# Kernel tuning notes

Hardware: AMD Instinct MI355X
Metric: run time of the kernel (lower is better)

## Reference

```python
import jax, jax.numpy as jnp
import numpy as np

N, E, D, H, ED = 50000, 150000, 128, 4, 16


def _ln(x, g, b, eps=1e-5):
    m = jnp.mean(x, -1, keepdims=True)
    v = jnp.var(x, -1, keepdims=True)
    return (x - m) / jnp.sqrt(v + eps) * g + b


def _seg_softmax(logits, seg, n):
    # numerically stable softmax over edges grouped by destination node
    m = jax.ops.segment_max(logits, seg, num_segments=n)
    e = jnp.exp(logits - m[seg])
    s = jax.ops.segment_sum(e, seg, num_segments=n)
    return e / (s[seg] + 1e-16)


def setup_inputs():
    key = jax.random.key(0)
    ks = jax.random.split(key, 16)
    def w(i, shape, s=0.05):
        return jax.random.normal(ks[i], shape, jnp.float32) * s
    return dict(
        x=w(0, (N, D), 1.0),
        edge_index=jax.random.randint(ks[1], (2, E), 0, N),
        edge_attr=w(2, (E, ED), 1.0),
        sage_Wl=w(3, (D, D)), sage_Wr=w(4, (D, D)), sage_b=jnp.zeros((D,), jnp.float32),
        tq_W=w(5, (D, H * D)), tq_b=jnp.zeros((H * D,), jnp.float32),
        tk_W=w(6, (D, H * D)), tk_b=jnp.zeros((H * D,), jnp.float32),
        tv_W=w(7, (D, H * D)), tv_b=jnp.zeros((H * D,), jnp.float32),
        te_W=w(8, (ED, H * D)),
        tskip_W=w(9, (D, D)), tskip_b=jnp.zeros((D,), jnp.float32),
        gat_W=w(10, (D, H * D)), gat_att_src=w(11, (H, D)), gat_att_dst=w(12, (H, D)),
        gat_bias=jnp.zeros((D,), jnp.float32),
        gate_short=jnp.ones((1,), jnp.float32), gate_attn=jnp.ones((1,), jnp.float32),
        gate_neighbor=jnp.ones((1,), jnp.float32),
        fus_W=w(13, (3 * D, D)), fus_b=jnp.zeros((D,), jnp.float32),
        fus_g=jnp.ones((D,), jnp.float32), fus_beta=jnp.zeros((D,), jnp.float32),
        norm_g=jnp.ones((D,), jnp.float32), norm_b=jnp.zeros((D,), jnp.float32),
    )


def reference(x, edge_index, edge_attr, sage_Wl, sage_Wr, sage_b,
              tq_W, tq_b, tk_W, tk_b, tv_W, tv_b, te_W, tskip_W, tskip_b,
              gat_W, gat_att_src, gat_att_dst, gat_bias,
              gate_short, gate_attn, gate_neighbor,
              fus_W, fus_b, fus_g, fus_beta, norm_g, norm_b):
    n, d = x.shape
    h = tq_W.shape[1] // d
    src, dst = edge_index[0], edge_index[1]

    # --- SAGEConv: mean aggregation of neighbors + root linear ---
    agg = jax.ops.segment_sum(x[src], dst, num_segments=n)
    cnt = jax.ops.segment_sum(jnp.ones((src.shape[0],), x.dtype), dst, num_segments=n)
    mean = agg / jnp.maximum(cnt, 1.0)[:, None]
    x_short = jax.nn.relu(mean @ sage_Wl + x @ sage_Wr + sage_b)

    # --- TransformerConv (concat=False, edge-conditioned key/value, skip) ---
    q = (x @ tq_W + tq_b).reshape(n, h, d)
    k = (x @ tk_W + tk_b).reshape(n, h, d)
    v = (x @ tv_W + tv_b).reshape(n, h, d)
    e = (edge_attr @ te_W).reshape(-1, h, d)           # [E,H,d]
    logits = jnp.sum(q[dst] * (k[src] + e), -1) / np.float32(np.sqrt(d))  # [E,H]
    alpha = _seg_softmax(logits, dst, n)
    out_t = jax.ops.segment_sum((v[src] + e) * alpha[..., None], dst, num_segments=n).mean(1)
    x_attn = jax.nn.relu(out_t + x @ tskip_W + tskip_b)

    # --- GATConv (adds self-loops, concat=False averages heads, bias) ---
    loops = jnp.arange(n)
    s2 = jnp.concatenate([src, loops])
    d2 = jnp.concatenate([dst, loops])
    g = (x @ gat_W).reshape(n, h, d)
    a_s = jnp.sum(g * gat_att_src, -1)                 # [N,H]
    a_d = jnp.sum(g * gat_att_dst, -1)
    lg = jax.nn.leaky_relu(a_s[s2] + a_d[d2], 0.2)     # [E+N,H]
    al = _seg_softmax(lg, d2, n)
    out_g = jax.ops.segment_sum(g[s2] * al[..., None], d2, num_segments=n).mean(1) + gat_bias
    x_nb = jax.nn.relu(out_g)

    # --- gated fusion + residual LayerNorm ---
    gs = jax.nn.sigmoid(gate_short)
    ga = jax.nn.sigmoid(gate_attn)
    gn = jax.nn.sigmoid(gate_neighbor)
    cat = jnp.concatenate([x_short * gs, x_attn * ga, x_nb * gn], -1)
    fused = jax.nn.relu(_ln(cat @ fus_W + fus_b, fus_g, fus_beta))
    return _ln(x + fused, norm_g, norm_b)
```

## Files before the change

kernel.cpp:

```cpp
#include <hip/hip_runtime.h>
#include <hip/hip_bf16.h>

using bf16 = __hip_bfloat16;
typedef __attribute__((ext_vector_type(8))) short short8;
typedef __attribute__((ext_vector_type(4))) float f32x4;
typedef __attribute__((ext_vector_type(4))) unsigned short u16x4;

__device__ __forceinline__ void store4(bf16* p, float v0, float v1, float v2, float v3) {
    u16x4 pk;
    bf16 h0 = __float2bfloat16(v0); pk[0] = *(unsigned short*)&h0;
    bf16 h1 = __float2bfloat16(v1); pk[1] = *(unsigned short*)&h1;
    bf16 h2 = __float2bfloat16(v2); pk[2] = *(unsigned short*)&h2;
    bf16 h3 = __float2bfloat16(v3); pk[3] = *(unsigned short*)&h3;
    *(u16x4*)p = pk;
}
__device__ __forceinline__ float b2f(short s) { bf16 h; *(short*)&h = s; return __bfloat162float(h); }

__device__ __forceinline__ void ld_lds16(void* lds, const void* g) {
    __builtin_amdgcn_global_load_lds(
        (const __attribute__((address_space(1))) unsigned int*)g,
        (__attribute__((address_space(3))) unsigned int*)lds,
        16, 0, 0);
}

__device__ __forceinline__ size_t pidx(int c, int k, int K) {
    return ((size_t)(((c >> 6) * (K >> 5) + (k >> 5)) * 4 + ((c >> 4) & 3)) * 64
            + (((k >> 3) & 3) * 16 + (c & 15))) * 8 + (k & 7);
}

__global__ __launch_bounds__(256) void zero_ws(unsigned* p, size_t n) {
    size_t i = (size_t)blockIdx.x * 256 + threadIdx.x;
    size_t stride = (size_t)gridDim.x * 256;
    for (; i < n; i += stride) p[i] = 0u;
}

__global__ __launch_bounds__(256) void prep_all(
    const float* __restrict__ x, bf16* __restrict__ x_b,
    bf16* __restrict__ Wt_sage, const float* __restrict__ sage_Wl, const float* __restrict__ sage_Wr,
    bf16* __restrict__ Wt_fus, const float* __restrict__ fus_W,
    const float* __restrict__ gate_s, const float* __restrict__ gate_a, const float* __restrict__ gate_n,
    bf16* __restrict__ Wt_cat, const float* __restrict__ tvW,
    const float* __restrict__ tskipW, const float* __restrict__ teW,
    bf16* __restrict__ Wgag, const float* __restrict__ gatW,
    float* __restrict__ bvsum, const float* __restrict__ tvb, int ND)
{
    const int TP = 128 * 128;
    long i = (long)blockIdx.x * 256 + threadIdx.x;
    long nv = ND >> 3;
    if (i < nv) {
        long b = i * 8;
        f32x4 a0 = *(const f32x4*)(x + b);
        f32x4 a1 = *(const f32x4*)(x + b + 4);
        short8 o;
        #pragma unroll
        for (int j = 0; j < 4; ++j) { bf16 h = __float2bfloat16(a0[j]); o[j] = *(short*)&h; }
        #pragma unroll
        for (int j = 0; j < 4; ++j) { bf16 h = __float2bfloat16(a1[j]); o[4 + j] = *(short*)&h; }
        *(short8*)(x_b + b) = o;
        return;
    }
    i -= nv;
    if (i < TP) { int k = (int)i / 128, c = (int)i % 128; Wt_sage[pidx(c, k, 256)] = __float2bfloat16(sage_Wl[i]); return; }
    i -= TP;
    if (i < TP) { int k = (int)i / 128, c = (int)i % 128; Wt_sage[pidx(c, k + 128, 256)] = __float2bfloat16(sage_Wr[i]); return; }
    i -= TP;
    if (i < 3 * TP) {
        int sseg = (int)(i / TP); int r = (int)(i % TP);
        int k = r / 128, c = r % 128;
        const float* g = sseg == 0 ? gate_s : (sseg == 1 ? gate_a : gate_n);
        float gv = 1.0f / (1.0f + expf(-g[0]));
        Wt_fus[pidx(c, sseg * 128 + k, 384)] = __float2bfloat16(fus_W[(size_t)sseg * TP + r] * gv);
        return;
    }
    i -= 3L * TP;
    if (i < 128L * 704) {
        int d = (int)(i / 704), kk = (int)(i % 704);
        float v;
        if (kk < 512)      { int h = kk >> 7, k = kk & 127; v = 0.25f * tvW[k * 512 + h * 128 + d]; }
        else if (kk < 640) { int k = kk - 512;              v = tskipW[k * 128 + d]; }
        else               { int t = kk - 640; int h = t >> 4, j = t & 15; v = 0.25f * teW[j * 512 + h * 128 + d]; }
        Wt_cat[pidx(d, kk, 704)] = __float2bfloat16(v);
        return;
    }
    i -= 128L * 704;
    if (i < 128L * 512) {
        int d = (int)i >> 9, k = (int)i & 511;
        int h = k >> 7, i2 = k & 127;
        Wgag[pidx(d, k, 512)] = __float2bfloat16(0.25f * gatW[(size_t)i2 * 512 + h * 128 + d]);
        return;
    }
    i -= 128L * 512;
    if (i < 128) {
        int d = (int)i;
        bvsum[d] = 0.25f * (tvb[d] + tvb[128 + d] + tvb[256 + d] + tvb[384 + d]);
    }
}

__global__ __launch_bounds__(128) void build_wbig(
    bf16* __restrict__ Wbig, float* __restrict__ bbig,
    const float* __restrict__ Wq, const float* __restrict__ Wk,
    const float* __restrict__ teW, const float* __restrict__ bq,
    const float* __restrict__ bk, const float* __restrict__ gatW,
    const float* __restrict__ attS, const float* __restrict__ attD)
{
    int c = blockIdx.x;
    int ip = threadIdx.x;
    float acc = 0.f, bacc = 0.f;
    if (c < 512) {
        int h = c >> 7, i2 = c & 127;
        const float* wkrow = Wk + (size_t)i2 * 512 + h * 128;
        const float* wqrow = Wq + (size_t)ip * 512 + h * 128;
        for (int o = 0; o < 128; ++o) acc += wqrow[o] * wkrow[o];
        if (ip == 0) { const float* bqr = bq + h * 128; for (int o = 0; o < 128; ++o) bacc += bqr[o] * wkrow[o]; }
    } else if (c < 576) {
        int t = c - 512; int h = t >> 4, j = t & 15;
        const float* terow = teW + (size_t)j * 512 + h * 128;
        const float* wqrow = Wq + (size_t)ip * 512 + h * 128;
        for (int o = 0; o < 128; ++o) acc += wqrow[o] * terow[o];
        if (ip == 0) { const float* bqr = bq + h * 128; for (int o = 0; o < 128; ++o) bacc += bqr[o] * terow[o]; }
    } else if (c < 580) {
        int h = c - 576;
        const float* bkr = bk + h * 128;
        const float* wqrow = Wq + (size_t)ip * 512 + h * 128;
        for (int o = 0; o < 128; ++o) acc += wqrow[o] * bkr[o];
        if (ip == 0) { const float* bqr = bq + h * 128; for (int o = 0; o < 128; ++o) bacc += bqr[o] * bkr[o]; }
    } else if (c < 584) {
        int h = c - 580;
        const float* ar = attS + h * 128;
        const float* gr = gatW + (size_t)ip * 512 + h * 128;
        for (int d = 0; d < 128; ++d) acc += gr[d] * ar[d];
    } else if (c < 588) {
        int h = c - 584;
        const float* ar = attD + h * 128;
        const float* gr = gatW + (size_t)ip * 512 + h * 128;
        for (int d = 0; d < 128; ++d) acc += gr[d] * ar[d];
    }
    Wbig[pidx(c, ip, 128)] = __float2bfloat16(acc);
    if (ip == 0) bbig[c] = bacc;
}

__global__ __launch_bounds__(256) void k_hist(const int* __restrict__ dst, int* __restrict__ deg_i, int E) {
    int e = blockIdx.x * 256 + threadIdx.x;
    if (e < E) atomicAdd(&deg_i[dst[e]], 1);
}

__global__ __launch_bounds__(256) void k_scan1(
    const int* __restrict__ deg_i, int* __restrict__ loc, int* __restrict__ partial, int N)
{
    __shared__ int sm[256];
    int t = threadIdx.x, i = blockIdx.x * 256 + t;
    int v = (i < N) ? deg_i[i] : 0;
    sm[t] = v;
    __syncthreads();
    for (int off = 1; off < 256; off <<= 1) {
        int add = (t >= off) ? sm[t - off] : 0;
        __syncthreads();
        sm[t] += add;
        __syncthreads();
    }
    if (i < N) loc[i] = sm[t] - v;
    if (t == 255) partial[blockIdx.x] = sm[255];
}

__global__ __launch_bounds__(256) void k_scan2(int* __restrict__ partial, int nb) {
    __shared__ int sm[256];
    int t = threadIdx.x;
    int v = (t < nb) ? partial[t] : 0;
    sm[t] = v;
    __syncthreads();
    for (int off = 1; off < 256; off <<= 1) {
        int add = (t >= off) ? sm[t - off] : 0;
        __syncthreads();
        sm[t] += add;
        __syncthreads();
    }
    if (t < nb) partial[t] = sm[t] - v;
}

__global__ __launch_bounds__(256) void k_scan3(
    const int* __restrict__ loc, const int* __restrict__ partial,
    int* __restrict__ rowptr, int* __restrict__ cursor, int N)
{
    int i = blockIdx.x * 256 + threadIdx.x;
    if (i >= N) return;
    int r = loc[i] + partial[blockIdx.x];
    rowptr[i] = r;
    cursor[i] = r;
}

__global__ __launch_bounds__(256) void k_scatter(
    const int* __restrict__ src, const int* __restrict__ dst,
    int* __restrict__ cursor, int* __restrict__ col_src, int* __restrict__ eidx, int E)
{
    int e = blockIdx.x * 256 + threadIdx.x;
    if (e >= E) return;
    int d = dst[e];
    int pos = atomicAdd(&cursor[d], 1);
    col_src[pos] = src[e];
    eidx[pos] = e;
}

__global__ __launch_bounds__(128) void gemm_wide(
    const bf16* __restrict__ A, const bf16* __restrict__ Wt,
    const float* __restrict__ bias, bf16* __restrict__ C, int n_rows, int ldc)
{
    int row0 = blockIdx.x * 64;
    int wave = threadIdx.x >> 6, lane = threadIdx.x & 63;
    int lrow = lane & 15, quad = lane >> 4;
    short8 xb[4][4];
    #pragma unroll
    for (int ks = 0; ks < 4; ++ks)
        #pragma unroll
        for (int nt = 0; nt < 4; ++nt) {
            int r = row0 + nt * 16 + lrow;
            r = r < n_rows ? r : n_rows - 1;
            xb[ks][nt] = *(const short8*)(A + (size_t)r * 128 + ks * 32 + quad * 8);
        }
    int c64 = blockIdx.y * 2 + wave;
    int cbase = c64 * 64;
    f32x4 acc[4][4] = {};
    #pragma unroll
    for (int ks = 0; ks < 4; ++ks) {
        short8 wf[4];
        #pragma unroll
        for (int mt = 0; mt < 4; ++mt)
            wf[mt] = *(const short8*)(Wt + ((size_t)((c64 * 4 + ks) * 4 + mt) * 64 + lane) * 8);
        #pragma unroll
        for (int mt = 0; mt < 4; ++mt)
            #pragma unroll
            for (int nt = 0; nt < 4; ++nt)
                acc[mt][nt] = __builtin_amdgcn_mfma_f32_16x16x32_bf16(wf[mt], xb[ks][nt], acc[mt][nt], 0, 0, 0);
    }
    #pragma unroll
    for (int nt = 0; nt < 4; ++nt) {
        int row = row0 + nt * 16 + lrow;
        if (row >= n_rows) continue;
        #pragma unroll
        for (int mt = 0; mt < 4; ++mt) {
            int col = cbase + mt * 16 + quad * 4;
            float b0 = 0.f, b1 = 0.f, b2 = 0.f, b3 = 0.f;
            if (bias) { b0 = bias[col]; b1 = bias[col + 1]; b2 = bias[col + 2]; b3 = bias[col + 3]; }
            store4(&C[(size_t)row * ldc + col],
                   acc[mt][nt][0] + b0, acc[mt][nt][1] + b1,
                   acc[mt][nt][2] + b2, acc[mt][nt][3] + b3);
        }
    }
}

#define NCAP 8
__global__ __launch_bounds__(256) void node_fused(
    const bf16* __restrict__ QT, const bf16* __restrict__ x_b,
    const float* __restrict__ edge_attr,
    const int* __restrict__ rowptr, const int* __restrict__ deg_i,
    const int* __restrict__ col_src, const int* __restrict__ eidx,
    bf16* __restrict__ mean_b, bf16* __restrict__ xa, bf16* __restrict__ ga,
    bf16* __restrict__ ea_b, int N)
{
    __shared__ short8 xS[4][NCAP][16];
    __shared__ float eaS[4][NCAP][16];
    __shared__ float wTs[4][NCAP][4];
    __shared__ float wGs[4][NCAP][4];
    int w = threadIdx.x >> 6, l = threadIdx.x & 63;
    int n = blockIdx.x * 4 + w;
    if (n >= N) return;
    int j = l & 15, g4 = l >> 4;
    int p0 = rowptr[n], dg = deg_i[n];
    const float scale = 0.08838834764831845f;
    float qtF[4][8], qeqL[4], qbL[4], adh[4], ashn[4];
    #pragma unroll
    for (int h = 0; h < 4; ++h) {
        short8 q = *(const short8*)(QT + (size_t)n * 640 + h * 128 + j * 8);
        #pragma unroll
        for (int t = 0; t < 8; ++t) qtF[h][t] = b2f(q[t]);
        qeqL[h] = __bfloat162float(QT[(size_t)n * 640 + 512 + h * 16 + j]);
        qbL[h]  = __bfloat162float(QT[(size_t)n * 640 + 576 + h]);
        ashn[h] = __bfloat162float(QT[(size_t)n * 640 + 580 + h]);
        adh[h]  = __bfloat162float(QT[(size_t)n * 640 + 584 + h]);
    }
    float xn0 = __bfloat162float(x_b[(size_t)n * 128 + l]);
    float xn1 = __bfloat162float(x_b[(size_t)n * 128 + l + 64]);
    float s_t[4], s_g[4], xaacc[8] = {}, gaacc[8];
    float mean0 = 0.f, mean1 = 0.f, eaacc = 0.f;
    #pragma unroll
    for (int h = 0; h < 4; ++h) {
        s_t[h] = 0.f;
        float lgs = ashn[h] + adh[h];
        lgs = lgs > 0.f ? lgs : 0.2f * lgs;
        float e = __expf(lgs);
        s_g[h] = e;
        gaacc[h * 2] = e * xn0; gaacc[h * 2 + 1] = e * xn1;
    }
    for (int c0 = 0; c0 < dg; c0 += NCAP) {
        int cc = min(NCAP, dg - c0);
        for (int it = 0; it < ((cc + 3) >> 2); ++it) {
            int i = it * 4 + g4;
            bool valid = i < cc;
            int s = 0;
            short8 xf = {0, 0, 0, 0, 0, 0, 0, 0};
            float ea_j = 0.f;
            if (valid) {
                s = col_src[p0 + c0 + i];
                int eg = eidx[p0 + c0 + i];
                xf = *(const short8*)(x_b + (size_t)s * 128 + j * 8);
                ea_j = edge_attr[(size_t)eg * 16 + j];
                xS[w][i][j] = xf;
                eaS[w][i][j] = ea_j;
            }
            float xv[8];
            #pragma unroll
            for (int t = 0; t < 8; ++t) xv[t] = b2f(xf[t]);
            float p[4];
            #pragma unroll
            for (int h = 0; h < 4; ++h) {
                float a = ea_j * qeqL[h];
                #pragma unroll
                for (int t = 0; t < 8; ++t) a += xv[t] * qtF[h][t];
                p[h] = a;
            }
            #pragma unroll
            for (int off = 1; off < 16; off <<= 1)
                #pragma unroll
                for (int h = 0; h < 4; ++h)
                    p[h] += __shfl_xor(p[h], off, 64);
            if (valid && j == 0) {
                #pragma unroll
                for (int h = 0; h < 4; ++h) {
                    wTs[w][i][h] = __expf((p[h] + qbL[h]) * scale);
                    float as_s = __bfloat162float(QT[(size_t)s * 640 + 580 + h]);
                    float lg = as_s + adh[h];
                    lg = lg > 0.f ? lg : 0.2f * lg;
                    wGs[w][i][h] = __expf(lg);
                }
            }
        }
        for (int i = 0; i < cc; ++i) {
            const bf16* xr = (const bf16*)&xS[w][i][0];
            float xv0 = __bfloat162float(xr[l]);
            float xv1 = __bfloat162float(xr[l + 64]);
            mean0 += xv0; mean1 += xv1;
            #pragma unroll
            for (int h = 0; h < 4; ++h) {
                float at = wTs[w][i][h], ag = wGs[w][i][h];
                s_t[h] += at; s_g[h] += ag;
                xaacc[h * 2] += at * xv0; xaacc[h * 2 + 1] += at * xv1;
                gaacc[h * 2] += ag * xv0; gaacc[h * 2 + 1] += ag * xv1;
            }
            eaacc += wTs[w][i][g4] * eaS[w][i][j];
        }
    }
    float invd = 1.f / fmaxf((float)dg, 1.f);
    mean_b[(size_t)n * 128 + l]      = __float2bfloat16(mean0 * invd);
    mean_b[(size_t)n * 128 + l + 64] = __float2bfloat16(mean1 * invd);
    #pragma unroll
    for (int h = 0; h < 4; ++h) {
        float it = 1.f / (s_t[h] + 1e-16f);
        xa[(size_t)n * 512 + h * 128 + l]      = __float2bfloat16(xaacc[h * 2] * it);
        xa[(size_t)n * 512 + h * 128 + l + 64] = __float2bfloat16(xaacc[h * 2 + 1] * it);
        float ig = 1.f / (s_g[h] + 1e-16f);
        ga[(size_t)n * 512 + h * 128 + l]      = __float2bfloat16(gaacc[h * 2] * ig);
        ga[(size_t)n * 512 + h * 128 + l + 64] = __float2bfloat16(gaacc[h * 2 + 1] * ig);
    }
    ea_b[(size_t)n * 64 + l] = __float2bfloat16(eaacc / (s_t[g4] + 1e-16f));
}

#define STASH(BIASP, USE_BV) do { \
    _Pragma("unroll") \
    for (int nt = 0; nt < 4; ++nt) { \
        int row_l = nt * 16 + lrow; \
        int sw = (row_l & 7) << 4; \
        float bvf = (USE_BV) ? ((deg_i[rA[nt]] > 0) ? 1.f : 0.f) : 0.f; \
        _Pragma("unroll") \
        for (int mt = 0; mt < 4; ++mt) { \
            int col = cbase + mt * 16 + quad * 4; \
            f32x4 bb = *(const f32x4*)((BIASP) + col); \
            u16x4 pk; \
            _Pragma("unroll") \
            for (int jj = 0; jj < 4; ++jj) { \
                float v = acc[mt][nt][jj] + bb[jj]; \
                if (USE_BV) v += bvf * bvsum[col + jj]; \
                bf16 h = __float2bfloat16(fmaxf(v, 0.f)); \
                pk[jj] = *(unsigned short*)&h; \
            } \
            *(u16x4*)(tileb + row_l * 256 + ((col * 2) ^ sw)) = pk; \
        } \
    } \
} while (0)

__global__ __launch_bounds__(128) void tail_fused(
    const bf16* __restrict__ mean_b, const bf16* __restrict__ x_b,
    const bf16* __restrict__ ga, const bf16* __restrict__ xa,
    const bf16* __restrict__ ea_b, const int* __restrict__ deg_i,
    const float* __restrict__ x,
    const bf16* __restrict__ Wt_sage, const bf16* __restrict__ Wgag,
    const bf16* __restrict__ Wt_cat, const bf16* __restrict__ Wt_fus,
    const float* __restrict__ sage_b, const float* __restrict__ gat_bias,
    const float* __restrict__ tskip_b, const float* __restrict__ bvsum,
    const float* __restrict__ fus_b, const float* __restrict__ fus_g,
    const float* __restrict__ fus_beta, const float* __restrict__ norm_g,
    const float* __restrict__ norm_b,
    float* __restrict__ out, int N)
{
    __shared__ __align__(16) char tileb[64 * 256];
    __shared__ __align__(16) short8 stg[2][2][8][64];
    __shared__ float2 st1[2][64];
    __shared__ float2 st2[2][64];
    int wave = threadIdx.x >> 6, lane = threadIdx.x & 63;
    int lrow = lane & 15, quad = lane >> 4;
    int kq = quad * 8;
    int row0 = blockIdx.x * 64;
    int cbase = wave * 64;
    int rA[4];
    #pragma unroll
    for (int t = 0; t < 4; ++t) {
        int r = row0 + t * 16 + lrow;
        rA[t] = r < N ? r : N - 1;
    }
    f32x4 facc[4][4] = {};

    auto issueA = [&](const bf16* base, int ldA, int kA, int par) {
        #pragma unroll
        for (int t = 0; t < 4; ++t)
            ld_lds16(&stg[wave][par][t][0], base + (size_t)rA[t] * ldA + kA);
    };
    auto issueW = [&](const bf16* Wt, int stepIdx, int par) {
        #pragma unroll
        for (int mt = 0; mt < 4; ++mt)
            ld_lds16(&stg[wave][par][4 + mt][0], Wt + ((size_t)(stepIdx * 4 + mt) * 64 + lane) * 8);
    };
    auto mfstep = [&](f32x4 (&acc)[4][4], int par) {
        short8 xf[4], wf[4];
        #pragma unroll
        for (int t = 0; t < 4; ++t) { xf[t] = stg[wave][par][t][lane]; wf[t] = stg[wave][par][4 + t][lane]; }
        #pragma unroll
        for (int mt = 0; mt < 4; ++mt)
            #pragma unroll
            for (int nt = 0; nt < 4; ++nt)
                acc[mt][nt] = __builtin_amdgcn_mfma_f32_16x16x32_bf16(wf[mt], xf[nt], acc[mt][nt], 0, 0, 0);
    };
    auto fuse_seg = [&](int SEG) {
        issueW(Wt_fus, wave * 12 + SEG * 4, 0);
        issueW(Wt_fus, wave * 12 + SEG * 4 + 1, 1);
        #pragma unroll
        for (int ks = 0; ks < 4; ++ks) {
            int cur = ks & 1;
            if (ks < 3) asm volatile("s_waitcnt vmcnt(4)" ::: "memory");
            else        asm volatile("s_waitcnt vmcnt(0)" ::: "memory");
            int kT = ks * 32 + kq;
            short8 xf[4], wf[4];
            #pragma unroll
            for (int t = 0; t < 4; ++t) {
                int row_l = t * 16 + lrow;
                xf[t] = *(const short8*)(tileb + row_l * 256 + ((kT * 2) ^ ((row_l & 7) << 4)));
            }
            #pragma unroll
            for (int mt = 0; mt < 4; ++mt) wf[mt] = stg[wave][cur][4 + mt][lane];
            #pragma unroll
            for (int mt = 0; mt < 4; ++mt)
                #pragma unroll
                for (int nt = 0; nt < 4; ++nt)
                    facc[mt][nt] = __builtin_amdgcn_mfma_f32_16x16x32_bf16(wf[mt], xf[nt], facc[mt][nt], 0, 0, 0);
            if (ks + 2 < 4) {
                asm volatile("s_waitcnt lgkmcnt(0)" ::: "memory");
                issueW(Wt_fus, wave * 12 + SEG * 4 + ks + 2, cur);
            }
        }
    };

    {
        f32x4 acc[4][4] = {};
        issueA(mean_b, 128, kq, 0);
        issueW(Wt_sage, wave * 8, 0);
        issueA(mean_b, 128, 32 + kq, 1);
        issueW(Wt_sage, wave * 8 + 1, 1);
        #pragma unroll
        for (int ks = 0; ks < 8; ++ks) {
            int cur = ks & 1;
            if (ks < 7) asm volatile("s_waitcnt vmcnt(8)" ::: "memory");
            else        asm volatile("s_waitcnt vmcnt(0)" ::: "memory");
            mfstep(acc, cur);
            if (ks + 2 < 8) {
                asm volatile("s_waitcnt lgkmcnt(0)" ::: "memory");
                int p = ks + 2;
                issueA((p < 4) ? mean_b : x_b, 128, (p & 3) * 32 + kq, cur);
                issueW(Wt_sage, wave * 8 + p, cur);
            }
        }
        STASH(sage_b, 0);
    }
    __syncthreads();
    fuse_seg(0);
    __syncthreads();

    {
        f32x4 acc[4][4] = {};
        issueA(xa, 512, kq, 0);
        issueW(Wt_cat, wave * 22, 0);
        issueA(xa, 512, 32 + kq, 1);
        issueW(Wt_cat, wave * 22 + 1, 1);
        #pragma unroll
        for (int ks = 0; ks < 22; ++ks) {
            int cur = ks & 1;
            if (ks < 21) asm volatile("s_waitcnt vmcnt(8)" ::: "memory");
            else         asm volatile("s_waitcnt vmcnt(0)" ::: "memory");
            mfstep(acc, cur);
            if (ks + 2 < 22) {
                asm volatile("s_waitcnt lgkmcnt(0)" ::: "memory");
                int p = ks + 2;
                if (p < 16)      issueA(xa,   512, p * 32 + kq,        cur);
                else if (p < 20) issueA(x_b,  128, (p - 16) * 32 + kq, cur);
                else             issueA(ea_b,  64, (p - 20) * 32 + kq, cur);
                issueW(Wt_cat, wave * 22 + p, cur);
            }
        }
        STASH(tskip_b, 1);
    }
    __syncthreads();
    fuse_seg(1);
    __syncthreads();

    {
        f32x4 acc[4][4] = {};
        issueA(ga, 512, kq, 0);
        issueW(Wgag, wave * 16, 0);
        issueA(ga, 512, 32 + kq, 1);
        issueW(Wgag, wave * 16 + 1, 1);
        #pragma unroll
        for (int ks = 0; ks < 16; ++ks) {
            int cur = ks & 1;
            if (ks < 15) asm volatile("s_waitcnt vmcnt(8)" ::: "memory");
            else         asm volatile("s_waitcnt vmcnt(0)" ::: "memory");
            mfstep(acc, cur);
            if (ks + 2 < 16) {
                asm volatile("s_waitcnt lgkmcnt(0)" ::: "memory");
                int p = ks + 2;
                issueA(ga, 512, p * 32 + kq, cur);
                issueW(Wgag, wave * 16 + p, cur);
            }
        }
        STASH(gat_bias, 0);
    }
    __syncthreads();
    fuse_seg(2);

    #pragma unroll
    for (int nt = 0; nt < 4; ++nt) {
        float s = 0.f, q = 0.f;
        #pragma unroll
        for (int mt = 0; mt < 4; ++mt) {
            int col = cbase + mt * 16 + quad * 4;
            f32x4 bb = *(const f32x4*)(fus_b + col);
            #pragma unroll
            for (int jj = 0; jj < 4; ++jj) {
                float v = facc[mt][nt][jj] + bb[jj];
                facc[mt][nt][jj] = v;
                s += v; q += v * v;
            }
        }
        s += __shfl_xor(s, 16, 64); q += __shfl_xor(q, 16, 64);
        s += __shfl_xor(s, 32, 64); q += __shfl_xor(q, 32, 64);
        if (quad == 0) st1[wave][nt * 16 + lrow] = make_float2(s, q);
    }
    __syncthreads();
    float m1[4], inv1[4];
    #pragma unroll
    for (int nt = 0; nt < 4; ++nt) {
        float2 a = st1[0][nt * 16 + lrow], b = st1[1][nt * 16 + lrow];
        float S = a.x + b.x, Q = a.y + b.y;
        float m = S * (1.f / 128.f);
        m1[nt] = m;
        inv1[nt] = rsqrtf(Q * (1.f / 128.f) - m * m + 1e-5f);
    }
    #pragma unroll
    for (int nt = 0; nt < 4; ++nt) {
        float s = 0.f, q = 0.f;
        #pragma unroll
        for (int mt = 0; mt < 4; ++mt) {
            int col = cbase + mt * 16 + quad * 4;
            f32x4 gv = *(const f32x4*)(fus_g + col);
            f32x4 bv = *(const f32x4*)(fus_beta + col);
            f32x4 xv = *(const f32x4*)(x + (size_t)rA[nt] * 128 + col);
            #pragma unroll
            for (int jj = 0; jj < 4; ++jj) {
                float y = fmaxf((facc[mt][nt][jj] - m1[nt]) * inv1[nt] * gv[jj] + bv[jj], 0.f);
                float z = xv[jj] + y;
                facc[mt][nt][jj] = z;
                s += z; q += z * z;
            }
        }
        s += __shfl_xor(s, 16, 64); q += __shfl_xor(q, 16, 64);
        s += __shfl_xor(s, 32, 64); q += __shfl_xor(q, 32, 64);
        if (quad == 0) st2[wave][nt * 16 + lrow] = make_float2(s, q);
    }
    __syncthreads();
    #pragma unroll
    for (int nt = 0; nt < 4; ++nt) {
        int row = row0 + nt * 16 + lrow;
        if (row >= N) continue;
        float2 a = st2[0][nt * 16 + lrow], b = st2[1][nt * 16 + lrow];
        float S = a.x + b.x, Q = a.y + b.y;
        float m = S * (1.f / 128.f);
        float inv = rsqrtf(Q * (1.f / 128.f) - m * m + 1e-5f);
        #pragma unroll
        for (int mt = 0; mt < 4; ++mt) {
            int col = cbase + mt * 16 + quad * 4;
            f32x4 ngv = *(const f32x4*)(norm_g + col);
            f32x4 nbv = *(const f32x4*)(norm_b + col);
            f32x4 o;
            #pragma unroll
            for (int jj = 0; jj < 4; ++jj)
                o[jj] = (facc[mt][nt][jj] - m) * inv * ngv[jj] + nbv[jj];
            *(f32x4*)(out + (size_t)row * 128 + col) = o;
        }
    }
}

extern "C" void kernel_launch(void* const* d_in, const int* in_sizes, int n_in,
                              void* d_out, int out_size, void* d_ws, size_t ws_size,
                              hipStream_t stream)
{
    const float* x        = (const float*)d_in[0];
    const int*   ei       = (const int*)d_in[1];
    const float* edge_attr= (const float*)d_in[2];
    const float* sage_Wl  = (const float*)d_in[3];
    const float* sage_Wr  = (const float*)d_in[4];
    const float* sage_b   = (const float*)d_in[5];
    const float* tq_W     = (const float*)d_in[6];
    const float* tq_b     = (const float*)d_in[7];
    const float* tk_W     = (const float*)d_in[8];
    const float* tk_b     = (const float*)d_in[9];
    const float* tv_W     = (const float*)d_in[10];
    const float* tv_b     = (const float*)d_in[11];
    const float* te_W     = (const float*)d_in[12];
    const float* tskip_W  = (const float*)d_in[13];
    const float* tskip_b  = (const float*)d_in[14];
    const float* gat_W    = (const float*)d_in[15];
    const float* att_s_w  = (const float*)d_in[16];
    const float* att_d_w  = (const float*)d_in[17];
    const float* gat_bias = (const float*)d_in[18];
    const float* gate_s   = (const float*)d_in[19];
    const float* gate_a   = (const float*)d_in[20];
    const float* gate_n   = (const float*)d_in[21];
    const float* fus_W    = (const float*)d_in[22];
    const float* fus_b    = (const float*)d_in[23];
    const float* fus_g    = (const float*)d_in[24];
    const float* fus_beta = (const float*)d_in[25];
    const float* norm_g   = (const float*)d_in[26];
    const float* norm_b   = (const float*)d_in[27];

    int N = in_sizes[0] / 128;
    int E = in_sizes[2] / 16;
    const int* src = ei;
    const int* dst = ei + E;
    int ND = N * 128;
    int nb = (N + 255) / 256;

    char* wsb = (char*)d_ws;
    size_t off = 0;
    auto carve = [&](size_t bytes) -> char* {
        char* p = wsb + off;
        off += (bytes + 255) & ~(size_t)255;
        return p;
    };
    int*   deg_i   = (int*)carve((size_t)N * 4);
    size_t zero_bytes = off;
    int*   rowptr  = (int*)carve((size_t)N * 4);
    int*   cursor  = (int*)carve((size_t)N * 4);
    int*   loc     = (int*)carve((size_t)N * 4);
    int*   partial = (int*)carve((size_t)256 * 4);
    int*   col_src = (int*)carve((size_t)E * 4);
    int*   eidx    = (int*)carve((size_t)E * 4);
    bf16*  x_b     = (bf16*)carve((size_t)N * 128 * 2);
    bf16*  QT      = (bf16*)carve((size_t)N * 640 * 2);
    bf16*  xa      = (bf16*)carve((size_t)N * 512 * 2);
    bf16*  ga      = (bf16*)carve((size_t)N * 512 * 2);
    bf16*  mean_b  = (bf16*)carve((size_t)N * 128 * 2);
    bf16*  ea_b    = (bf16*)carve((size_t)N * 64 * 2);
    bf16*  Wbig    = (bf16*)carve((size_t)640 * 128 * 2);
    float* bbig    = (float*)carve((size_t)640 * 4);
    bf16*  Wt_sage = (bf16*)carve((size_t)128 * 256 * 2);
    bf16*  Wt_fus  = (bf16*)carve((size_t)128 * 384 * 2);
    bf16*  Wt_cat  = (bf16*)carve((size_t)128 * 704 * 2);
    bf16*  Wgag    = (bf16*)carve((size_t)128 * 512 * 2);
    float* bvsum   = (float*)carve((size_t)128 * 4);

    zero_ws<<<256, 256, 0, stream>>>((unsigned*)wsb, zero_bytes / 4);
    const long TP = 128 * 128;
    long prep_total = (long)(ND >> 3) + 5L * TP + 128L * 704 + 128L * 512 + 128;
    int prep_blocks = (int)((prep_total + 255) / 256);
    prep_all<<<prep_blocks, 256, 0, stream>>>(
        x, x_b, Wt_sage, sage_Wl, sage_Wr, Wt_fus, fus_W, gate_s, gate_a, gate_n,
        Wt_cat, tv_W, tskip_W, te_W, Wgag, gat_W, bvsum, tv_b, ND);
    build_wbig<<<640, 128, 0, stream>>>(Wbig, bbig, tq_W, tk_W, te_W, tq_b, tk_b,
                                        gat_W, att_s_w, att_d_w);

    k_hist<<<(E + 255) / 256, 256, 0, stream>>>(dst, deg_i, E);
    k_scan1<<<nb, 256, 0, stream>>>(deg_i, loc, partial, N);
    k_scan2<<<1, 256, 0, stream>>>(partial, nb);
    k_scan3<<<nb, 256, 0, stream>>>(loc, partial, rowptr, cursor, N);
    k_scatter<<<(E + 255) / 256, 256, 0, stream>>>(src, dst, cursor, col_src, eidx, E);

    int gy64 = (N + 63) / 64, gnode = (N + 3) / 4;

    gemm_wide<<<dim3(gy64, 5), 128, 0, stream>>>(x_b, Wbig, bbig, QT, N, 640);

    node_fused<<<gnode, 256, 0, stream>>>(QT, x_b, edge_attr, rowptr, deg_i, col_src, eidx,
                                          mean_b, xa, ga, ea_b, N);

    tail_fused<<<gy64, 128, 0, stream>>>(
        mean_b, x_b, ga, xa, ea_b, deg_i, x,
        Wt_sage, Wgag, Wt_cat, Wt_fus,
        sage_b, gat_bias, tskip_b, bvsum,
        fus_b, fus_g, fus_beta, norm_g, norm_b,
        (float*)d_out, N);
}
```

Baseline: 373.4 us.

## Fold weight-build and zeroing into prep kernel; loop gemm_wide over column tiles with LDS prefetch

The separate zero_ws and build_wbig launches are removed. Their work, the Wbig/bbig fold and zeroing the degree histogram, now runs as extra index ranges inside prep_all, which cuts two kernel launches. gemm_wide now uses a 1D grid: each block keeps its x fragments in registers and loops over all five 128-column groups. Weight tiles are double-buffered into LDS with global_load_lds and manual waitcnt. This reuses the A loads across column groups and hides weight fetch latency, at the cost of fewer blocks, less parallelism and per-thread serial dot products now inside prep_all.

```diff
diff --git a/kernel.cpp b/kernel.cpp
--- a/kernel.cpp
+++ b/kernel.cpp
@@ -26,12 +26,6 @@
 __device__ __forceinline__ size_t pidx(int c, int k, int K) {
     return ((size_t)(((c >> 6) * (K >> 5) + (k >> 5)) * 4 + ((c >> 4) & 3)) * 64
             + (((k >> 3) & 3) * 16 + (c & 15))) * 8 + (k & 7);
-}
-
-__global__ __launch_bounds__(256) void zero_ws(unsigned* p, size_t n) {
-    size_t i = (size_t)blockIdx.x * 256 + threadIdx.x;
-    size_t stride = (size_t)gridDim.x * 256;
-    for (; i < n; i += stride) p[i] = 0u;
 }
 
 __global__ __launch_bounds__(256) void prep_all(
@@ -42,7 +36,12 @@
     bf16* __restrict__ Wt_cat, const float* __restrict__ tvW,
     const float* __restrict__ tskipW, const float* __restrict__ teW,
     bf16* __restrict__ Wgag, const float* __restrict__ gatW,
-    float* __restrict__ bvsum, const float* __restrict__ tvb, int ND)
+    float* __restrict__ bvsum, const float* __restrict__ tvb,
+    bf16* __restrict__ Wbig, float* __restrict__ bbig,
+    const float* __restrict__ Wq, const float* __restrict__ Wk,
+    const float* __restrict__ bq, const float* __restrict__ bk,
+    const float* __restrict__ attS, const float* __restrict__ attD,
+    int* __restrict__ deg_i, int N, int ND)
 {
     const int TP = 128 * 128;
     long i = (long)blockIdx.x * 256 + threadIdx.x;
@@ -93,57 +92,57 @@
     if (i < 128) {
         int d = (int)i;
         bvsum[d] = 0.25f * (tvb[d] + tvb[128 + d] + tvb[256 + d] + tvb[384 + d]);
-    }
-}
-
-__global__ __launch_bounds__(128) void build_wbig(
-    bf16* __restrict__ Wbig, float* __restrict__ bbig,
-    const float* __restrict__ Wq, const float* __restrict__ Wk,
-    const float* __restrict__ teW, const float* __restrict__ bq,
-    const float* __restrict__ bk, const float* __restrict__ gatW,
-    const float* __restrict__ attS, const float* __restrict__ attD)
-{
-    int c = blockIdx.x;
-    int ip = threadIdx.x;
-    float acc = 0.f, bacc = 0.f;
-    if (c < 512) {
-        int h = c >> 7, i2 = c & 127;
-        const float* wkrow = Wk + (size_t)i2 * 512 + h * 128;
-        const float* wqrow = Wq + (size_t)ip * 512 + h * 128;
-        for (int o = 0; o < 128; ++o) acc += wqrow[o] * wkrow[o];
-        if (ip == 0) { const float* bqr = bq + h * 128; for (int o = 0; o < 128; ++o) bacc += bqr[o] * wkrow[o]; }
-    } else if (c < 576) {
-        int t = c - 512; int h = t >> 4, j = t & 15;
-        const float* terow = teW + (size_t)j * 512 + h * 128;
-        const float* wqrow = Wq + (size_t)ip * 512 + h * 128;
-        for (int o = 0; o < 128; ++o) acc += wqrow[o] * terow[o];
-        if (ip == 0) { const float* bqr = bq + h * 128; for (int o = 0; o < 128; ++o) bacc += bqr[o] * terow[o]; }
-    } else if (c < 580) {
-        int h = c - 576;
-        const float* bkr = bk + h * 128;
-        const float* wqrow = Wq + (size_t)ip * 512 + h * 128;
-        for (int o = 0; o < 128; ++o) acc += wqrow[o] * bkr[o];
-        if (ip == 0) { const float* bqr = bq + h * 128; for (int o = 0; o < 128; ++o) bacc += bqr[o] * bkr[o]; }
-    } else if (c < 584) {
-        int h = c - 580;
-        const float* ar = attS + h * 128;
-        const float* gr = gatW + (size_t)ip * 512 + h * 128;
-        for (int d = 0; d < 128; ++d) acc += gr[d] * ar[d];
-    } else if (c < 588) {
-        int h = c - 584;
-        const float* ar = attD + h * 128;
-        const float* gr = gatW + (size_t)ip * 512 + h * 128;
-        for (int d = 0; d < 128; ++d) acc += gr[d] * ar[d];
-    }
-    Wbig[pidx(c, ip, 128)] = __float2bfloat16(acc);
-    if (ip == 0) bbig[c] = bacc;
+        return;
+    }
+    i -= 128;
+    if (i < 640L * 128) {
+        int c = (int)(i >> 7), ip = (int)(i & 127);
+        float acc = 0.f, bacc = 0.f;
+        if (c < 512) {
+            int h = c >> 7, i2 = c & 127;
+            const float* wkrow = Wk + (size_t)i2 * 512 + h * 128;
+            const float* wqrow = Wq + (size_t)ip * 512 + h * 128;
+            for (int o = 0; o < 128; ++o) acc += wqrow[o] * wkrow[o];
+            if (ip == 0) { const float* bqr = bq + h * 128; for (int o = 0; o < 128; ++o) bacc += bqr[o] * wkrow[o]; }
+        } else if (c < 576) {
+            int t = c - 512; int h = t >> 4, j = t & 15;
+            const float* terow = teW + (size_t)j * 512 + h * 128;
+            const float* wqrow = Wq + (size_t)ip * 512 + h * 128;
+            for (int o = 0; o < 128; ++o) acc += wqrow[o] * terow[o];
+            if (ip == 0) { const float* bqr = bq + h * 128; for (int o = 0; o < 128; ++o) bacc += bqr[o] * terow[o]; }
+        } else if (c < 580) {
+            int h = c - 576;
+            const float* bkr = bk + h * 128;
+            const float* wqrow = Wq + (size_t)ip * 512 + h * 128;
+            for (int o = 0; o < 128; ++o) acc += wqrow[o] * bkr[o];
+            if (ip == 0) { const float* bqr = bq + h * 128; for (int o = 0; o < 128; ++o) bacc += bqr[o] * bkr[o]; }
+        } else if (c < 584) {
+            int h = c - 580;
+            const float* ar = attS + h * 128;
+            const float* gr = gatW + (size_t)ip * 512 + h * 128;
+            for (int d = 0; d < 128; ++d) acc += gr[d] * ar[d];
+        } else if (c < 588) {
+            int h = c - 584;
+            const float* ar = attD + h * 128;
+            const float* gr = gatW + (size_t)ip * 512 + h * 128;
+            for (int d = 0; d < 128; ++d) acc += gr[d] * ar[d];
+        }
+        Wbig[pidx(c, ip, 128)] = __float2bfloat16(acc);
+        if (ip == 0) bbig[c] = bacc;
+        return;
+    }
+    i -= 640L * 128;
+    long z = i * 4;
+    if (z < N) {
+        if (z + 4 <= N) { *(int4*)(deg_i + z) = make_int4(0, 0, 0, 0); }
+        else { for (long zz = z; zz < N; ++zz) deg_i[zz] = 0; }
+    }
 }
 
 __global__ __launch_bounds__(256) void k_hist(const int* __restrict__ dst, int* __restrict__ deg_i, int E) {
     int e = blockIdx.x * 256 + threadIdx.x;
     if (e < E) atomicAdd(&deg_i[dst[e]], 1);
 }
-
 __global__ __launch_bounds__(256) void k_scan1(
     const int* __restrict__ deg_i, int* __restrict__ loc, int* __restrict__ partial, int N)
 {
@@ -161,7 +160,6 @@
     if (i < N) loc[i] = sm[t] - v;
     if (t == 255) partial[blockIdx.x] = sm[255];
 }
-
 __global__ __launch_bounds__(256) void k_scan2(int* __restrict__ partial, int nb) {
     __shared__ int sm[256];
     int t = threadIdx.x;
@@ -176,7 +174,6 @@
     }
     if (t < nb) partial[t] = sm[t] - v;
 }
-
 __global__ __launch_bounds__(256) void k_scan3(
     const int* __restrict__ loc, const int* __restrict__ partial,
     int* __restrict__ rowptr, int* __restrict__ cursor, int N)
@@ -187,7 +184,6 @@
     rowptr[i] = r;
     cursor[i] = r;
 }
-
 __global__ __launch_bounds__(256) void k_scatter(
     const int* __restrict__ src, const int* __restrict__ dst,
     int* __restrict__ cursor, int* __restrict__ col_src, int* __restrict__ eidx, int E)
@@ -204,6 +200,7 @@
     const bf16* __restrict__ A, const bf16* __restrict__ Wt,
     const float* __restrict__ bias, bf16* __restrict__ C, int n_rows, int ldc)
 {
+    __shared__ __align__(16) short8 wstg[2][2][4][64];
     int row0 = blockIdx.x * 64;
     int wave = threadIdx.x >> 6, lane = threadIdx.x & 63;
     int lrow = lane & 15, quad = lane >> 4;
@@ -216,33 +213,47 @@
             r = r < n_rows ? r : n_rows - 1;
             xb[ks][nt] = *(const short8*)(A + (size_t)r * 128 + ks * 32 + quad * 8);
         }
-    int c64 = blockIdx.y * 2 + wave;
-    int cbase = c64 * 64;
-    f32x4 acc[4][4] = {};
-    #pragma unroll
-    for (int ks = 0; ks < 4; ++ks) {
-        short8 wf[4];
+    auto issueW = [&](int s, int par) {
+        int c64 = (s >> 2) * 2 + wave, ks = s & 3;
         #pragma unroll
         for (int mt = 0; mt < 4; ++mt)
-            wf[mt] = *(const short8*)(Wt + ((size_t)((c64 * 4 + ks) * 4 + mt) * 64 + lane) * 8);
-        #pragma unroll
-        for (int mt = 0; mt < 4; ++mt)
-            #pragma unroll
-            for (int nt = 0; nt < 4; ++nt)
-                acc[mt][nt] = __builtin_amdgcn_mfma_f32_16x16x32_bf16(wf[mt], xb[ks][nt], acc[mt][nt], 0, 0, 0);
-    }
-    #pragma unroll
-    for (int nt = 0; nt < 4; ++nt) {
-        int row = row0 + nt * 16 + lrow;
-        if (row >= n_rows) continue;
-        #pragma unroll
-        for (int mt = 0; mt < 4; ++mt) {
-            int col = cbase + mt * 16 + quad * 4;
-            float b0 = 0.f, b1 = 0.f, b2 = 0.f, b3 = 0.f;
-            if (bias) { b0 = bias[col]; b1 = bias[col + 1]; b2 = bias[col + 2]; b3 = bias[col + 3]; }
-            store4(&C[(size_t)row * ldc + col],
-                   acc[mt][nt][0] + b0, acc[mt][nt][1] + b1,
-                   acc[mt][nt][2] + b2, acc[mt][nt][3] + b3);
+            ld_lds16(&wstg[wave][par][mt][0], Wt + ((size_t)((c64 * 4 + ks) * 4 + mt) * 64 + lane) * 8);
+    };
+    issueW(0, 0);
+    issueW(1, 1);
+    for (int cy = 0; cy < 5; ++cy) {
+        f32x4 acc[4][4] = {};
+        #pragma unroll
+        for (int ks = 0; ks < 4; ++ks) {
+            int s = cy * 4 + ks, par = s & 1;
+            if (s < 18) asm volatile("s_waitcnt vmcnt(4)" ::: "memory");
+            else        asm volatile("s_waitcnt vmcnt(0)" ::: "memory");
+            short8 wf[4];
+            #pragma unroll
+            for (int mt = 0; mt < 4; ++mt) wf[mt] = wstg[wave][par][mt][lane];
+            asm volatile("s_waitcnt lgkmcnt(0)" ::: "memory");
+            if (s + 2 < 20) issueW(s + 2, par);
+            __builtin_amdgcn_sched_barrier(0);
+            #pragma unroll
+            for (int mt = 0; mt < 4; ++mt)
+                #pragma unroll
+                for (int nt = 0; nt < 4; ++nt)
+                    acc[mt][nt] = __builtin_amdgcn_mfma_f32_16x16x32_bf16(wf[mt], xb[ks][nt], acc[mt][nt], 0, 0, 0);
+        }
+        int cbase = (cy * 2 + wave) * 64;
+        #pragma unroll
+        for (int nt = 0; nt < 4; ++nt) {
+            int row = row0 + nt * 16 + lrow;
+            if (row >= n_rows) continue;
+            #pragma unroll
+            for (int mt = 0; mt < 4; ++mt) {
+                int col = cbase + mt * 16 + quad * 4;
+                float b0 = 0.f, b1 = 0.f, b2 = 0.f, b3 = 0.f;
+                if (bias) { b0 = bias[col]; b1 = bias[col + 1]; b2 = bias[col + 2]; b3 = bias[col + 3]; }
+                store4(&C[(size_t)row * ldc + col],
+                       acc[mt][nt][0] + b0, acc[mt][nt][1] + b1,
+                       acc[mt][nt][2] + b2, acc[mt][nt][3] + b3);
+            }
         }
     }
 }
@@ -662,7 +673,6 @@
         return p;
     };
     int*   deg_i   = (int*)carve((size_t)N * 4);
-    size_t zero_bytes = off;
     int*   rowptr  = (int*)carve((size_t)N * 4);
     int*   cursor  = (int*)carve((size_t)N * 4);
     int*   loc     = (int*)carve((size_t)N * 4);
@@ -683,15 +693,15 @@
     bf16*  Wgag    = (bf16*)carve((size_t)128 * 512 * 2);
     float* bvsum   = (float*)carve((size_t)128 * 4);
 
-    zero_ws<<<256, 256, 0, stream>>>((unsigned*)wsb, zero_bytes / 4);
     const long TP = 128 * 128;
-    long prep_total = (long)(ND >> 3) + 5L * TP + 128L * 704 + 128L * 512 + 128;
+    long prep_total = (long)(ND >> 3) + 5L * TP + 128L * 704 + 128L * 512 + 128
+                    + 640L * 128 + ((long)N + 3) / 4;
     int prep_blocks = (int)((prep_total + 255) / 256);
     prep_all<<<prep_blocks, 256, 0, stream>>>(
         x, x_b, Wt_sage, sage_Wl, sage_Wr, Wt_fus, fus_W, gate_s, gate_a, gate_n,
-        Wt_cat, tv_W, tskip_W, te_W, Wgag, gat_W, bvsum, tv_b, ND);
-    build_wbig<<<640, 128, 0, stream>>>(Wbig, bbig, tq_W, tk_W, te_W, tq_b, tk_b,
-                                        gat_W, att_s_w, att_d_w);
+        Wt_cat, tv_W, tskip_W, te_W, Wgag, gat_W, bvsum, tv_b,
+        Wbig, bbig, tq_W, tk_W, tq_b, tk_b, att_s_w, att_d_w,
+        deg_i, N, ND);
 
     k_hist<<<(E + 255) / 256, 256, 0, stream>>>(dst, deg_i, E);
     k_scan1<<<nb, 256, 0, stream>>>(deg_i, loc, partial, N);
@@ -701,7 +711,7 @@
 
     int gy64 = (N + 63) / 64, gnode = (N + 3) / 4;
 
-    gemm_wide<<<dim3(gy64, 5), 128, 0, stream>>>(x_b, Wbig, bbig, QT, N, 640);
+    gemm_wide<<<gy64, 128, 0, stream>>>(x_b, Wbig, bbig, QT, N, 640);
 
     node_fused<<<gnode, 256, 0, stream>>>(QT, x_b, edge_attr, rowptr, deg_i, col_src, eidx,
                                           mean_b, xa, ga, ea_b, N);
```

After: 376.3 us. About the same (+0.8%).
